# Kernel tuning notes

Measured on AMD Instinct MI355X. Metric: run time of the kernel, lower is better.

## Reference

```python
import jax, jax.numpy as jnp
import numpy as np

NUM_GRAPHS = 128

def _gcn_conv(x, W, b, src, dst, deg_inv_sqrt, n_nodes):
    # PyG GCNConv: h = X W; out[dst] += d^-1/2[src] * d^-1/2[dst] * h[src]; out += b
    h = x @ W
    norm = deg_inv_sqrt[src] * deg_inv_sqrt[dst]  # [E]
    msg = h[src] * norm[:, None]                  # [E, C]
    out = jax.ops.segment_sum(msg, dst, num_segments=n_nodes)
    return out + b


def setup_inputs() -> dict:
    key = jax.random.key(0)
    k1, k2, k3, k4, k5 = jax.random.split(key, 5)
    n_nodes, n_edges, c_in, c_hid = 50000, 800000, 256, 256
    x = jax.random.normal(k1, (n_nodes, c_in), dtype=jnp.float32)
    edge_index = jax.random.randint(k2, (2, n_edges), 0, n_nodes, dtype=jnp.int64)
    batch = jnp.sort(jax.random.randint(k3, (n_nodes,), 0, NUM_GRAPHS, dtype=jnp.int64))
    s1 = 1.0 / np.sqrt(c_in)
    s2 = 1.0 / np.sqrt(c_hid)
    W1 = jax.random.uniform(k4, (c_in, c_hid), jnp.float32, -s1, s1)
    b1 = jnp.zeros((c_hid,), jnp.float32)
    W2 = jax.random.uniform(k5, (c_hid, c_hid), jnp.float32, -s2, s2)
    b2 = jnp.zeros((c_hid,), jnp.float32)
    return {"x": x, "edge_index": edge_index, "batch": batch,
            "W1": W1, "b1": b1, "W2": W2, "b2": b2}


def reference(x, edge_index, batch, W1, b1, W2, b2):
    n_nodes = x.shape[0]
    # add self-loops (GCNConv default add_self_loops=True)
    loops = jnp.arange(n_nodes, dtype=edge_index.dtype)
    src = jnp.concatenate([edge_index[0], loops])
    dst = jnp.concatenate([edge_index[1], loops])
    deg = jax.ops.segment_sum(jnp.ones_like(dst, dtype=x.dtype), dst, num_segments=n_nodes)
    deg_inv_sqrt = jnp.where(deg > 0, jax.lax.rsqrt(deg), 0.0)

    h = jax.nn.relu(_gcn_conv(x, W1, b1, src, dst, deg_inv_sqrt, n_nodes))
    # dropout p=0.2 is identity in eval mode
    h = jax.nn.relu(_gcn_conv(h, W2, b2, src, dst, deg_inv_sqrt, n_nodes))

    # global mean pool over graph ids
    sums = jax.ops.segment_sum(h, batch, num_segments=NUM_GRAPHS)
    cnts = jax.ops.segment_sum(jnp.ones((n_nodes,), h.dtype), batch, num_segments=NUM_GRAPHS)
    return sums / jnp.maximum(cnts, 1.0)[:, None]
```

## Files before the change

kernel.cpp:

```cpp
#include <hip/hip_runtime.h>

#define NCH 256
#define NS  16

typedef short short8 __attribute__((ext_vector_type(8)));
typedef float f32x4  __attribute__((ext_vector_type(4)));

__device__ __forceinline__ float b2f(unsigned short u) {
    union { unsigned int i; float f; } x; x.i = ((unsigned int)u) << 16; return x.f;
}
__device__ __forceinline__ unsigned short f2b(float f) {
    unsigned int u = __float_as_uint(f);
    unsigned int r = (u + 0x7FFFu + ((u >> 16) & 1u)) >> 16;
    return (unsigned short)r;
}

#define GLOAD_LDS16(gptr, lptr) \
    __builtin_amdgcn_global_load_lds((const __attribute__((address_space(1))) void*)(gptr), \
                                     (__attribute__((address_space(3))) void*)(lptr), 16, 0, 0)

__global__ __launch_bounds__(256) void k_pre(const int* __restrict__ dst, int E,
                                             int* __restrict__ deg, int nh,
                                             unsigned shmul,
                                             const float* __restrict__ W1,
                                             const float* __restrict__ W2,
                                             unsigned short* __restrict__ Wt1,
                                             unsigned short* __restrict__ Wt2) {
    int b = blockIdx.x;
    if (b < nh) {
        const int shard  = b & 7;
        const int nchunk = nh >> 3;
        const int chunk  = b >> 3;
        const int per = (E + nchunk - 1) / nchunk;
        const int e0 = chunk * per;
        const int e1 = min(e0 + per, E);
        for (int e = e0 + threadIdx.x; e < e1; e += 256) {
            int d = dst[e];
            if ((int)__umulhi((unsigned)d, shmul) == shard)
                atomicAdd(&deg[d], 1);
        }
    } else {
        int k = (b - nh) & 255;
        const float* W = ((b - nh) >> 8) ? W2 : W1;
        unsigned short* Wt = ((b - nh) >> 8) ? Wt2 : Wt1;
        int n = threadIdx.x;
        Wt[(size_t)n * 256 + k] = f2b(W[(size_t)k * 256 + n]);
    }
}

__global__ __launch_bounds__(256) void k_scan_blk(const int* __restrict__ deg,
                                                  int* __restrict__ part,
                                                  int* __restrict__ bsum, int N) {
    __shared__ int sm[256];
    int t = threadIdx.x;
    int base = blockIdx.x * 1024 + t * 4;
    int v[4]; int s = 0;
#pragma unroll
    for (int j = 0; j < 4; ++j) {
        int i = base + j;
        int d = (i < N) ? deg[i] : 0;
        v[j] = d; s += d;
    }
    sm[t] = s; __syncthreads();
#pragma unroll
    for (int off = 1; off < 256; off <<= 1) {
        int u = (t >= off) ? sm[t - off] : 0;
        __syncthreads();
        sm[t] += u;
        __syncthreads();
    }
    int excl = sm[t] - s;
#pragma unroll
    for (int j = 0; j < 4; ++j) {
        int i = base + j;
        if (i < N) part[i] = excl;
        excl += v[j];
    }
    if (t == 255) bsum[blockIdx.x] = sm[255];
}

__global__ void k_scan_top(int* __restrict__ bsum, int nb, int* __restrict__ rowptr_end) {
    int t = threadIdx.x;
    int orig = (t < nb) ? bsum[t] : 0;
    int v = orig;
#pragma unroll
    for (int off = 1; off < 64; off <<= 1) {
        int u = __shfl_up(v, off, 64);
        if (t >= off) v += u;
    }
    if (t < nb) bsum[t] = v - orig;
    if (t == 63) *rowptr_end = v;
}

__global__ __launch_bounds__(256) void k_finalize(const int* __restrict__ deg,
                                                  int* __restrict__ row_ptr,
                                                  const int* __restrict__ boff,
                                                  int* __restrict__ cursor,
                                                  float* __restrict__ dinv, int N) {
    int i = blockIdx.x * 256 + threadIdx.x;
    if (i < N) {
        int rp = row_ptr[i] + boff[i >> 10];
        row_ptr[i] = rp;
        cursor[i]  = rp;
        dinv[i] = rsqrtf((float)(deg[i] + 1));
    }
}

__global__ __launch_bounds__(256) void k_scatter_sh(const int* __restrict__ src,
                                                    const int* __restrict__ dst, int E,
                                                    int* __restrict__ cursor,
                                                    const float* __restrict__ dinv,
                                                    int2* __restrict__ cw,
                                                    unsigned shmul) {
    const int shard  = blockIdx.x & 7;
    const int nchunk = gridDim.x >> 3;
    const int chunk  = blockIdx.x >> 3;
    const int per = (E + nchunk - 1) / nchunk;
    const int e0 = chunk * per;
    const int e1 = min(e0 + per, E);
    for (int e = e0 + threadIdx.x; e < e1; e += 256) {
        int d = dst[e];
        int s = (int)__umulhi((unsigned)d, shmul);
        if (s == shard) {
            int sv = src[e];
            int pos = atomicAdd(&cursor[d], 1);
            cw[pos] = make_int2(sv, __float_as_int(dinv[sv]));
        }
    }
}

__device__ __forceinline__ void load_bfr(const unsigned short* __restrict__ Bt,
                                         short8 bfr[2][8], int w, int lr, int ku) {
    const unsigned short* pb = Bt + (size_t)(w * 32 + lr) * NCH + ku * 8;
#pragma unroll
    for (int nf = 0; nf < 2; ++nf)
#pragma unroll
        for (int ks = 0; ks < 8; ++ks)
            bfr[nf][ks] = *(const short8*)(pb + nf * 16 * NCH + ks * 32);
}

__device__ __forceinline__ void gemm_compute_store(const unsigned short* As,
                                                   const short8 bfr[2][8],
                                                   unsigned short* __restrict__ C,
                                                   int M, int t, int w, int lr, int ku) {
    f32x4 acc[2][2];
#pragma unroll
    for (int rf = 0; rf < 2; ++rf)
#pragma unroll
        for (int nf = 0; nf < 2; ++nf) acc[rf][nf] = (f32x4){0.f, 0.f, 0.f, 0.f};

#pragma unroll
    for (int ks = 0; ks < 8; ++ks) {
#pragma unroll
        for (int rf = 0; rf < 2; ++rf) {
            int row = rf * 16 + lr;
            int uu  = (ks * 4 + ku) ^ (row & 7);
            short8 af = *(const short8*)&As[row * 256 + uu * 8];
            acc[rf][0] = __builtin_amdgcn_mfma_f32_16x16x32_bf16(bfr[0][ks], af,
                                                                 acc[rf][0], 0, 0, 0);
            acc[rf][1] = __builtin_amdgcn_mfma_f32_16x16x32_bf16(bfr[1][ks], af,
                                                                 acc[rf][1], 0, 0, 0);
        }
    }

#pragma unroll
    for (int rf = 0; rf < 2; ++rf) {
        int row = t * 32 + rf * 16 + lr;
        if (row < M) {
            unsigned short* pc = C + (size_t)row * NCH + w * 32 + ku * 4;
#pragma unroll
            for (int nf = 0; nf < 2; ++nf) {
                unsigned short us[4];
                us[0] = f2b(acc[rf][nf][0]); us[1] = f2b(acc[rf][nf][1]);
                us[2] = f2b(acc[rf][nf][2]); us[3] = f2b(acc[rf][nf][3]);
                *(int2*)(pc + nf * 16) = *(const int2*)us;
            }
        }
    }
}

__global__ __launch_bounds__(512, 4) void k_gemm2(const unsigned short* __restrict__ A,
                                                  const unsigned short* __restrict__ Bt,
                                                  unsigned short* __restrict__ C,
                                                  int M, int tiles) {
    __shared__ unsigned short As[2][32 * 256];
    const int tid  = threadIdx.x;
    const int w    = tid >> 6;
    const int lane = tid & 63;
    const int lr   = lane & 15;
    const int ku   = lane >> 4;

    short8 bfr[2][8];
    load_bfr(Bt, bfr, w, lr, ku);

    const int gu0 = w * 128 + lane;

#define STAGE2(tt, buf) do {                                                  \
        _Pragma("unroll")                                                     \
        for (int j = 0; j < 2; ++j) {                                         \
            int gu = gu0 + j * 64;                                            \
            int r  = gu >> 5;                                                 \
            int u  = gu & 31;                                                 \
            int grow = (tt) * 32 + r; if (grow >= M) grow = M - 1;            \
            const unsigned short* gp = A + (size_t)grow * NCH +               \
                                       ((u ^ (r & 7)) << 3);                  \
            GLOAD_LDS16(gp, (buf) + (size_t)(w * 128 + j * 64) * 8);          \
        }                                                                     \
    } while (0)

    int t = blockIdx.x;
    int cur = 0;
    if (t < tiles) STAGE2(t, As[0]);
    __syncthreads();

    for (; t < tiles; t += gridDim.x) {
        int tn = t + gridDim.x;
        if (tn < tiles) STAGE2(tn, As[cur ^ 1]);
        gemm_compute_store(As[cur], bfr, C, M, t, w, lr, ku);
        __syncthreads();
        cur ^= 1;
    }
#undef STAGE2
}

__global__ __launch_bounds__(512, 4) void k_gemm1(const float* __restrict__ A,
                                                  const unsigned short* __restrict__ Bt,
                                                  unsigned short* __restrict__ C,
                                                  int M, int tiles) {
    __shared__ unsigned short As[2][32 * 256];
    const int tid  = threadIdx.x;
    const int w    = tid >> 6;
    const int lane = tid & 63;
    const int lr   = lane & 15;
    const int ku   = lane >> 4;

    short8 bfr[2][8];
    load_bfr(Bt, bfr, w, lr, ku);

    const int r0_ = tid >> 5,          u0_ = tid & 31;
    const int r1_ = (tid + 512) >> 5,  u1_ = (tid + 512) & 31;

    int t = blockIdx.x;
    int cur = 0;
    if (t < tiles) {
        int g0 = t * 32 + r0_; if (g0 >= M) g0 = M - 1;
        int g1 = t * 32 + r1_; if (g1 >= M) g1 = M - 1;
        const float4* pa0 = (const float4*)(A + (size_t)g0 * NCH + u0_ * 8);
        const float4* pa1 = (const float4*)(A + (size_t)g1 * NCH + u1_ * 8);
        float4 a0 = pa0[0], a1 = pa0[1];
        float4 b0 = pa1[0], b1 = pa1[1];
        unsigned short us[8];
        us[0]=f2b(a0.x); us[1]=f2b(a0.y); us[2]=f2b(a0.z); us[3]=f2b(a0.w);
        us[4]=f2b(a1.x); us[5]=f2b(a1.y); us[6]=f2b(a1.z); us[7]=f2b(a1.w);
        *(int4*)&As[0][r0_ * 256 + ((u0_ ^ (r0_ & 7)) << 3)] = *(const int4*)us;
        us[0]=f2b(b0.x); us[1]=f2b(b0.y); us[2]=f2b(b0.z); us[3]=f2b(b0.w);
        us[4]=f2b(b1.x); us[5]=f2b(b1.y); us[6]=f2b(b1.z); us[7]=f2b(b1.w);
        *(int4*)&As[0][r1_ * 256 + ((u1_ ^ (r1_ & 7)) << 3)] = *(const int4*)us;
    }
    __syncthreads();

    for (; t < tiles; t += gridDim.x) {
        int tn = t + gridDim.x;
        float4 a0, a1, b0, b1;
        if (tn < tiles) {
            int g0 = tn * 32 + r0_; if (g0 >= M) g0 = M - 1;
            int g1 = tn * 32 + r1_; if (g1 >= M) g1 = M - 1;
            const float4* pa0 = (const float4*)(A + (size_t)g0 * NCH + u0_ * 8);
            const float4* pa1 = (const float4*)(A + (size_t)g1 * NCH + u1_ * 8);
            a0 = pa0[0]; a1 = pa0[1];
            b0 = pa1[0]; b1 = pa1[1];
        }

        gemm_compute_store(As[cur], bfr, C, M, t, w, lr, ku);

        if (tn < tiles) {
            unsigned short us[8];
            us[0]=f2b(a0.x); us[1]=f2b(a0.y); us[2]=f2b(a0.z); us[3]=f2b(a0.w);
            us[4]=f2b(a1.x); us[5]=f2b(a1.y); us[6]=f2b(a1.z); us[7]=f2b(a1.w);
            *(int4*)&As[cur ^ 1][r0_ * 256 + ((u0_ ^ (r0_ & 7)) << 3)] = *(const int4*)us;
            us[0]=f2b(b0.x); us[1]=f2b(b0.y); us[2]=f2b(b0.z); us[3]=f2b(b0.w);
            us[4]=f2b(b1.x); us[5]=f2b(b1.y); us[6]=f2b(b1.z); us[7]=f2b(b1.w);
            *(int4*)&As[cur ^ 1][r1_ * 256 + ((u1_ ^ (r1_ & 7)) << 3)] = *(const int4*)us;
        }
        __syncthreads();
        cur ^= 1;
    }
}

__global__ __launch_bounds__(256) void k_agg_w(const unsigned short* __restrict__ h,
                                               const float* __restrict__ dinv,
                                               const int* __restrict__ row_ptr,
                                               const int2* __restrict__ cw,
                                               const float* __restrict__ bias,
                                               unsigned short* __restrict__ out, int M) {
    int v = blockIdx.x * 4 + (threadIdx.x >> 6);
    if (v >= M) return;
    const int lane = threadIdx.x & 63;
    const int half = lane >> 5;
    const int cb   = (lane & 31) << 3;

    float acc[8] = {};
    float dv = dinv[v];

    short8 rs = {};
    if (half == 0) rs = *(const short8*)&h[(size_t)v * NCH + cb];

    int beg = row_ptr[v], end = row_ptr[v + 1];
    int i0 = beg + half * 2;

    short8 r0 = {}, r1 = {};
    float  w0 = 0.f, w1 = 0.f;
    bool b0 = i0 < end, b1 = i0 + 1 < end;
    if (b0) {
        int2 e = cw[i0];
        r0 = *(const short8*)&h[(size_t)e.x * NCH + cb];
        w0 = __int_as_float(e.y);
    }
    if (b1) {
        int2 e = cw[i0 + 1];
        r1 = *(const short8*)&h[(size_t)e.x * NCH + cb];
        w1 = __int_as_float(e.y);
    }

    while (b0) {
        int in = i0 + 4;
        bool n0 = in < end, n1 = in + 1 < end;
        short8 s0 = {}, s1 = {};
        float  x0 = 0.f, x1 = 0.f;
        if (n0) {
            int2 e = cw[in];
            s0 = *(const short8*)&h[(size_t)e.x * NCH + cb];
            x0 = __int_as_float(e.y);
        }
        if (n1) {
            int2 e = cw[in + 1];
            s1 = *(const short8*)&h[(size_t)e.x * NCH + cb];
            x1 = __int_as_float(e.y);
        }
#pragma unroll
        for (int i = 0; i < 8; ++i) acc[i] += w0 * b2f((unsigned short)r0[i]);
#pragma unroll
        for (int i = 0; i < 8; ++i) acc[i] += w1 * b2f((unsigned short)r1[i]);
        r0 = s0; r1 = s1; w0 = x0; w1 = x1; b0 = n0; b1 = n1; i0 = in;
    }

    if (half == 0) {
#pragma unroll
        for (int i = 0; i < 8; ++i) acc[i] += dv * b2f((unsigned short)rs[i]);
    }

#pragma unroll
    for (int i = 0; i < 8; ++i) acc[i] += __shfl_xor(acc[i], 32, 64);

    if (half == 0) {
        f32x4 bl = *(const f32x4*)&bias[cb];
        f32x4 bh = *(const f32x4*)&bias[cb + 4];
        unsigned short us[8];
#pragma unroll
        for (int i = 0; i < 8; ++i) {
            float b = (i < 4) ? bl[i] : bh[i - 4];
            us[i] = f2b(fmaxf(dv * acc[i] + b, 0.0f));
        }
        *(int4*)&out[(size_t)v * NCH + cb] = *(const int4*)us;
    }
}

__device__ __forceinline__ int lower_bound_i(const int* a, int n, int key) {
    int lo = 0, hi = n;
    while (lo < hi) {
        int mid = (lo + hi) >> 1;
        if (a[mid] < key) lo = mid + 1; else hi = mid;
    }
    return lo;
}

__global__ __launch_bounds__(64) void k_pool_a(const unsigned short* __restrict__ a,
                                               const int* __restrict__ batch,
                                               float* __restrict__ partial, int N) {
    int g = blockIdx.x, s = blockIdx.y;
    const int lane = threadIdx.x;
    const int half = lane >> 5;
    const int cb   = (lane & 31) << 3;

    int lo = lower_bound_i(batch, N, g);
    int hi = lower_bound_i(batch, N, g + 1);
    int cnt = hi - lo;
    int len = (cnt + NS - 1) / NS;
    int rlo = lo + s * len;
    int rhi = min(rlo + len, hi);

    float acc[8] = {};
    for (int r = rlo + half; r < rhi; r += 2) {
        short8 hv = *(const short8*)&a[(size_t)r * NCH + cb];
#pragma unroll
        for (int i = 0; i < 8; ++i) acc[i] += b2f((unsigned short)hv[i]);
    }
#pragma unroll
    for (int i = 0; i < 8; ++i) acc[i] += __shfl_xor(acc[i], 32, 64);

    if (half == 0) {
        float* p = partial + ((size_t)g * NS + s) * NCH + cb;
        *(f32x4*)p       = (f32x4){acc[0], acc[1], acc[2], acc[3]};
        *(f32x4*)(p + 4) = (f32x4){acc[4], acc[5], acc[6], acc[7]};
    }
}

__global__ __launch_bounds__(256) void k_pool_b(const float* __restrict__ partial,
                                                const int* __restrict__ batch,
                                                float* __restrict__ out, int N) {
    int g = blockIdx.x, ch = threadIdx.x;
    int lo = lower_bound_i(batch, N, g);
    int hi = lower_bound_i(batch, N, g + 1);
    float s = 0.0f;
#pragma unroll
    for (int k = 0; k < NS; ++k)
        s += partial[((size_t)g * NS + k) * NCH + ch];
    out[(size_t)g * NCH + ch] = s / (float)max(hi - lo, 1);
}

extern "C" void kernel_launch(void* const* d_in, const int* in_sizes, int n_in,
                              void* d_out, int out_size, void* d_ws, size_t ws_size,
                              hipStream_t stream) {
    const float* x     = (const float*)d_in[0];
    const int*   ei    = (const int*)d_in[1];
    const int*   batch = (const int*)d_in[2];
    const float* W1    = (const float*)d_in[3];
    const float* b1    = (const float*)d_in[4];
    const float* W2    = (const float*)d_in[5];
    const float* b2    = (const float*)d_in[6];
    float* out = (float*)d_out;

    const int M = in_sizes[0] / NCH;
    const int E = in_sizes[1] / 2;
    const int* src = ei;
    const int* dst = ei + E;

    char* w = (char*)d_ws;
    auto alloc = [&](size_t bytes) -> void* {
        void* p = (void*)w;
        w += (bytes + 255) & ~(size_t)255;
        return p;
    };
    int*   deg     = (int*)alloc((size_t)M * 4);
    float* dinv    = (float*)alloc((size_t)M * 4);
    int*   row_ptr = (int*)alloc((size_t)(M + 1) * 4);
    int*   cursor  = (int*)alloc((size_t)M * 4);
    int*   bsum    = (int*)alloc(64 * 4);
    int2*  cw      = (int2*)alloc((size_t)E * 8);
    unsigned short* bufP = (unsigned short*)alloc((size_t)M * NCH * 2);
    unsigned short* bufQ = (unsigned short*)alloc((size_t)M * NCH * 2);
    unsigned short* Wt1  = (unsigned short*)alloc((size_t)NCH * NCH * 2);
    unsigned short* Wt2  = (unsigned short*)alloc((size_t)NCH * NCH * 2);
    float* partial = (float*)alloc((size_t)128 * NS * NCH * 4);

    const int nb = (M + 1023) / 1024;
    const unsigned shmul = (unsigned)(((8ull << 32) + M - 1) / (unsigned long long)M);
    const int tiles = (M + 31) / 32;
    const int nh = 2048;

    (void)hipMemsetAsync(deg, 0, (size_t)M * 4, stream);
    k_pre<<<nh + 512, 256, 0, stream>>>(dst, E, deg, nh, shmul, W1, W2, Wt1, Wt2);
    k_scan_blk<<<nb, 256, 0, stream>>>(deg, row_ptr, bsum, M);
    k_scan_top<<<1, 64, 0, stream>>>(bsum, nb, row_ptr + M);
    k_finalize<<<(M + 255) / 256, 256, 0, stream>>>(deg, row_ptr, bsum, cursor, dinv, M);
    k_scatter_sh<<<4096, 256, 0, stream>>>(src, dst, E, cursor, dinv, cw, shmul);

    const int ggrid = 512;
    const int agrid = (M + 3) / 4;

    k_gemm1<<<ggrid, 512, 0, stream>>>(x, Wt1, bufP, M, tiles);
    k_agg_w<<<agrid, 256, 0, stream>>>(bufP, dinv, row_ptr, cw, b1, bufQ, M);
    k_gemm2<<<ggrid, 512, 0, stream>>>(bufQ, Wt2, bufP, M, tiles);
    k_agg_w<<<agrid, 256, 0, stream>>>(bufP, dinv, row_ptr, cw, b2, bufQ, M);
    k_pool_a<<<dim3(128, NS), 64, 0, stream>>>(bufQ, batch, partial, M);
    k_pool_b<<<128, 256, 0, stream>>>(partial, batch, out, M);
}
```

Baseline: 276.5 us.

## Fuse CSR edge scatter into first GEMM launch as extra blocks

Removes the separate scatter kernel and runs its work in extra blocks appended to the first GEMM launch. GEMM blocks keep striding over tiles by gblocks, while the scatter blocks fill the CSR edge array. The aim is to overlap the memory- and atomic-bound scatter with the compute-bound GEMM and save one launch. Scatter blocks now use 512 threads and carry the GEMM's shared-memory and register footprint, so they may limit occupancy and compete with GEMM blocks for CUs.

```diff
diff --git a/kernel.cpp b/kernel.cpp
--- a/kernel.cpp
+++ b/kernel.cpp
@@ -106,29 +106,6 @@
     }
 }
 
-__global__ __launch_bounds__(256) void k_scatter_sh(const int* __restrict__ src,
-                                                    const int* __restrict__ dst, int E,
-                                                    int* __restrict__ cursor,
-                                                    const float* __restrict__ dinv,
-                                                    int2* __restrict__ cw,
-                                                    unsigned shmul) {
-    const int shard  = blockIdx.x & 7;
-    const int nchunk = gridDim.x >> 3;
-    const int chunk  = blockIdx.x >> 3;
-    const int per = (E + nchunk - 1) / nchunk;
-    const int e0 = chunk * per;
-    const int e1 = min(e0 + per, E);
-    for (int e = e0 + threadIdx.x; e < e1; e += 256) {
-        int d = dst[e];
-        int s = (int)__umulhi((unsigned)d, shmul);
-        if (s == shard) {
-            int sv = src[e];
-            int pos = atomicAdd(&cursor[d], 1);
-            cw[pos] = make_int2(sv, __float_as_int(dinv[sv]));
-        }
-    }
-}
-
 __device__ __forceinline__ void load_bfr(const unsigned short* __restrict__ Bt,
                                          short8 bfr[2][8], int w, int lr, int ku) {
     const unsigned short* pb = Bt + (size_t)(w * 32 + lr) * NCH + ku * 8;
@@ -223,12 +200,39 @@
 #undef STAGE2
 }
 
-__global__ __launch_bounds__(512, 4) void k_gemm1(const float* __restrict__ A,
-                                                  const unsigned short* __restrict__ Bt,
-                                                  unsigned short* __restrict__ C,
-                                                  int M, int tiles) {
+__global__ __launch_bounds__(512, 4) void k_gemm1s(const float* __restrict__ A,
+                                                   const unsigned short* __restrict__ Bt,
+                                                   unsigned short* __restrict__ C,
+                                                   int M, int tiles, int gblocks,
+                                                   const int* __restrict__ src,
+                                                   const int* __restrict__ dst, int E,
+                                                   int* __restrict__ cursor,
+                                                   const float* __restrict__ dinv,
+                                                   int2* __restrict__ cw,
+                                                   unsigned shmul) {
     __shared__ unsigned short As[2][32 * 256];
-    const int tid  = threadIdx.x;
+    const int tid = threadIdx.x;
+
+    if (blockIdx.x >= gblocks) {
+        const int b = blockIdx.x - gblocks;
+        const int shard  = b & 7;
+        const int nchunk = (gridDim.x - gblocks) >> 3;
+        const int chunk  = b >> 3;
+        const int per = (E + nchunk - 1) / nchunk;
+        const int e0 = chunk * per;
+        const int e1 = min(e0 + per, E);
+        for (int e = e0 + tid; e < e1; e += 512) {
+            int d = dst[e];
+            int s = (int)__umulhi((unsigned)d, shmul);
+            if (s == shard) {
+                int sv = src[e];
+                int pos = atomicAdd(&cursor[d], 1);
+                cw[pos] = make_int2(sv, __float_as_int(dinv[sv]));
+            }
+        }
+        return;
+    }
+
     const int w    = tid >> 6;
     const int lane = tid & 63;
     const int lr   = lane & 15;
@@ -259,8 +263,8 @@
     }
     __syncthreads();
 
-    for (; t < tiles; t += gridDim.x) {
-        int tn = t + gridDim.x;
+    for (; t < tiles; t += gblocks) {
+        int tn = t + gblocks;
         float4 a0, a1, b0, b1;
         if (tn < tiles) {
             int g0 = tn * 32 + r0_; if (g0 >= M) g0 = M - 1;
@@ -457,20 +461,21 @@
     const unsigned shmul = (unsigned)(((8ull << 32) + M - 1) / (unsigned long long)M);
     const int tiles = (M + 31) / 32;
     const int nh = 2048;
+    const int gblocks = 512;
+    const int sblocks = 2048;
 
     (void)hipMemsetAsync(deg, 0, (size_t)M * 4, stream);
     k_pre<<<nh + 512, 256, 0, stream>>>(dst, E, deg, nh, shmul, W1, W2, Wt1, Wt2);
     k_scan_blk<<<nb, 256, 0, stream>>>(deg, row_ptr, bsum, M);
     k_scan_top<<<1, 64, 0, stream>>>(bsum, nb, row_ptr + M);
     k_finalize<<<(M + 255) / 256, 256, 0, stream>>>(deg, row_ptr, bsum, cursor, dinv, M);
-    k_scatter_sh<<<4096, 256, 0, stream>>>(src, dst, E, cursor, dinv, cw, shmul);
-
-    const int ggrid = 512;
+
     const int agrid = (M + 3) / 4;
 
-    k_gemm1<<<ggrid, 512, 0, stream>>>(x, Wt1, bufP, M, tiles);
+    k_gemm1s<<<gblocks + sblocks, 512, 0, stream>>>(x, Wt1, bufP, M, tiles, gblocks,
+                                                    src, dst, E, cursor, dinv, cw, shmul);
     k_agg_w<<<agrid, 256, 0, stream>>>(bufP, dinv, row_ptr, cw, b1, bufQ, M);
-    k_gemm2<<<ggrid, 512, 0, stream>>>(bufQ, Wt2, bufP, M, tiles);
+    k_gemm2<<<512, 512, 0, stream>>>(bufQ, Wt2, bufP, M, tiles);
     k_agg_w<<<agrid, 256, 0, stream>>>(bufP, dinv, row_ptr, cw, b2, bufQ, M);
     k_pool_a<<<dim3(128, NS), 64, 0, stream>>>(bufQ, batch, partial, M);
     k_pool_b<<<128, 256, 0, stream>>>(partial, batch, out, M);
```

Result: no change. 272.4 us (-1.5%).
